# Performance work log

Measured on AMD Instinct MI355X. Metric: run time of the kernel, lower is better.

## Reference

```python
import jax, jax.numpy as jnp
import numpy as np

EPS = 0.5          # entropy_epsilon
TAU = 0.5          # tau = 1 * entropy_epsilon
MAXITER = 10

NABLA_W = np.array([[[[0., 0., 0.], [0., -1., 0.], [0., 1., 0.]]],
                    [[[0., 0., 0.], [0., -1., 1.], [0., 0., 0.]]]], dtype=np.float32)  # (2,1,3,3)
DIV_W = np.array([[[[0., -1., 0.], [0., 1., 0.], [0., 0., 0.]],
                   [[0., 0., 0.], [-1., 1., 0.], [0., 0., 0.]]]], dtype=np.float32)    # (1,2,3,3)


def _conv(x, w):
    # x: (B,C,H,W), w: (O,I,3,3), padding=1 -> SAME
    return jax.lax.conv_general_dilated(
        x, w, window_strides=(1, 1), padding='SAME',
        dimension_numbers=('NCHW', 'OIHW', 'NCHW'))


def setup_inputs() -> dict:
    key = jax.random.key(0)
    k1, k2 = jax.random.split(key)
    B, H, W = 8, 1024, 1024
    o = jax.random.normal(k1, (B, 1, H, W), dtype=jnp.float32)
    vector_field = jax.random.normal(k2, (H, W, 2), dtype=jnp.float32)
    nabla_w = jnp.asarray(NABLA_W)
    div_w = jnp.asarray(DIV_W)
    return {"o": o, "vector_field": vector_field, "nabla_w": nabla_w, "div_w": div_w}


def reference(o, vector_field, nabla_w, div_w):
    o = o[:, 0]                      # (B,H,W)
    vf1 = vector_field[:, :, 1]      # (H,W)
    vf0 = vector_field[:, :, 0]      # (H,W)
    u = jax.nn.sigmoid(o / EPS)
    q = jnp.zeros_like(o)
    Tq = jnp.zeros_like(o)
    for _ in range(MAXITER):
        u_nabla = _conv(u[:, None], nabla_w)          # (B,2,H,W)
        q = q - TAU * (u_nabla[:, 0] * vf1 + u_nabla[:, 1] * vf0)
        q = jnp.maximum(q, 0.0)
        Tq = _conv(jnp.stack([vf1 * q, vf0 * q], axis=1), div_w)[:, 0]  # (B,H,W)
        u = jax.nn.sigmoid((o - Tq) / EPS)
    u1 = (o - Tq) / EPS
    return u1
```

## Files before the change

### kernel.cpp

```cpp
#include <hip/hip_runtime.h>
#include <math.h>

#define IMG_H 1024
#define IMG_W 1024
#define IMG_B 8
#define TPB 512
#define PXT 2
#define RPB 16
#define BANDS (IMG_H / RPB)
#define NBLK (IMG_B * BANDS)

__device__ __forceinline__ float sig2(float x) {
    return 1.0f / (1.0f + __expf(-2.0f * x));
}
__device__ __forceinline__ int imax(int a, int b) { return a > b ? a : b; }
__device__ __forceinline__ int imin(int a, int b) { return a < b ? a : b; }

template<int D, bool READQ, bool FINAL>
__global__ __launch_bounds__(TPB, 4) void k_pipe(const float* __restrict__ qin,
                                                 const float* __restrict__ vf,
                                                 const float* __restrict__ o,
                                                 float* __restrict__ out) {
    __shared__ float sp[D + 1][TPB + 1];
    __shared__ float su[D][2][TPB + 1];

    const int img = blockIdx.x / BANDS;
    const int r0  = (blockIdx.x % BANDS) * RPB;
    const int tid = threadIdx.x;
    const int x0  = tid * PXT;
    const size_t ibase = (size_t)img * IMG_H * IMG_W;

    if (tid == 0) {
#pragma unroll
        for (int l = 0; l <= D; ++l) sp[l][0] = 0.0f;
#pragma unroll
        for (int l = 0; l < D; ++l) { su[l][0][TPB] = 0.0f; su[l][1][TPB] = 0.0f; }
    }

    constexpr int HALO = FINAL ? 1 : 0;
    constexpr int NOH  = FINAL ? D + 1 : D;

    const int u0lo = imax(r0 - (D - 1) - HALO, 0);
    const int ylo  = READQ ? imax(r0 - D - HALO, 0) : u0lo;
    const int yend = r0 + RPB - 1 + D;
    const int yhi  = imin(yend, IMG_H - 1);

    float qc[PXT], qn[PXT], qz[PXT];
    float oh[NOH][PXT], on[PXT];
    float v0h[D + 1][PXT], v1h[D + 1][PXT], v0n[PXT], v1n[PXT];
    float uY[D][PXT], uZ[D][PXT];
    float p1prev[D + 1][PXT];
    float qsave[D][PXT];
    float qvPrev[PXT];

#pragma unroll
    for (int j = 0; j < PXT; ++j) {
        qc[j]=qn[j]=qz[j]=on[j]=v0n[j]=v1n[j]=qvPrev[j]=0.0f;
#pragma unroll
        for (int l = 0; l < NOH; ++l) oh[l][j] = 0.0f;
#pragma unroll
        for (int l = 0; l <= D; ++l) { v0h[l][j]=0.0f; v1h[l][j]=0.0f; p1prev[l][j]=0.0f; }
#pragma unroll
        for (int l = 0; l < D; ++l) { uY[l][j]=0.0f; uZ[l][j]=0.0f; qsave[l][j]=0.0f; }
    }

    {
        const size_t rb = ibase + (size_t)ylo * IMG_W + x0;
        if constexpr (READQ) {
            float2 q2 = *(const float2*)(qin + rb);
            qc[0]=q2.x; qc[1]=q2.y;
        }
        float2 o2 = *(const float2*)(o + rb);
        oh[0][0]=o2.x; oh[0][1]=o2.y;
        const size_t vb = ((size_t)ylo * IMG_W + x0) * 2;
        float4 va = *(const float4*)(vf + vb);
        v0h[0][0]=va.x; v1h[0][0]=va.y; v0h[0][1]=va.z; v1h[0][1]=va.w;
    }

    for (int y = ylo; y <= yend; ++y) {
        if (y + 1 <= yhi) {
            const size_t rb = ibase + (size_t)(y + 1) * IMG_W + x0;
            if constexpr (READQ) {
                float2 q2 = *(const float2*)(qin + rb);
                qn[0]=q2.x; qn[1]=q2.y;
            }
            float2 o2 = *(const float2*)(o + rb);
            on[0]=o2.x; on[1]=o2.y;
            const size_t vb = ((size_t)(y + 1) * IMG_W + x0) * 2;
            float4 va = *(const float4*)(vf + vb);
            v0n[0]=va.x; v1n[0]=va.y; v0n[1]=va.z; v1n[1]=va.w;
        } else {
#pragma unroll
            for (int j = 0; j < PXT; ++j) { qn[j]=0.f; on[j]=0.f; v0n[j]=0.f; v1n[j]=0.f; }
        }

        if constexpr (READQ) {
            float p0c[PXT], p1c[PXT];
            const bool haveY = (y <= yhi);
            if (haveY) {
#pragma unroll
                for (int j = 0; j < PXT; ++j) { p0c[j]=v0h[0][j]*qc[j]; p1c[j]=v1h[0][j]*qc[j]; }
                sp[0][tid + 1] = p0c[PXT - 1];
            } else {
#pragma unroll
                for (int j = 0; j < PXT; ++j) { p0c[j]=0.f; p1c[j]=0.f; }
            }
            __syncthreads();
            if (y >= u0lo) {
                const float lft = sp[0][tid];
#pragma unroll
                for (int j = 0; j < PXT; ++j) {
                    float pm1 = (j == 0) ? lft : p0c[j - 1];
                    float nu = (y <= IMG_H - 1)
                        ? sig2(oh[0][j] - (p1c[j] - p1prev[0][j] + p0c[j] - pm1)) : 0.0f;
                    uZ[0][j] = uY[0][j]; uY[0][j] = nu;
                }
                su[0][y & 1][tid] = uY[0][0];
            }
#pragma unroll
            for (int j = 0; j < PXT; ++j) p1prev[0][j] = p1c[j];
        } else {
#pragma unroll
            for (int j = 0; j < PXT; ++j) {
                float nu = (y <= IMG_H - 1) ? sig2(oh[0][j]) : 0.0f;
                uZ[0][j] = uY[0][j]; uY[0][j] = nu;
            }
            su[0][y & 1][tid] = uY[0][0];
        }

#pragma unroll
        for (int l = 1; l <= D; ++l) {
            const int t = y - l;
            const int qlo = imax(r0 - (D - l) - HALO, 0);
            const bool qvalid = (t >= qlo) && (t <= IMG_H - 1);
            float qbase[PXT], qv[PXT];
#pragma unroll
            for (int j = 0; j < PXT; ++j)
                qbase[j] = (l == 1) ? (READQ ? qz[j] : 0.0f) : qsave[l - 1][j];
            if (l >= 2) {
#pragma unroll
                for (int j = 0; j < PXT; ++j) qsave[l - 1][j] = qvPrev[j];
            }
            if (qvalid) {
                const float uR = su[l - 1][t & 1][tid + 1];
#pragma unroll
                for (int j = 0; j < PXT; ++j) {
                    float gy = uY[l - 1][j] - uZ[l - 1][j];
                    float gx = ((j < PXT - 1) ? uZ[l - 1][j + 1] : uR) - uZ[l - 1][j];
                    qv[j] = fmaxf(qbase[j] - 0.5f * (gy * v1h[l][j] + gx * v0h[l][j]), 0.0f);
                }
            } else {
#pragma unroll
                for (int j = 0; j < PXT; ++j) qv[j] = 0.0f;
            }

            if (l < D) {
                float p0p[PXT], p1p[PXT];
                if (qvalid) {
#pragma unroll
                    for (int j = 0; j < PXT; ++j) { p0p[j]=v0h[l][j]*qv[j]; p1p[j]=v1h[l][j]*qv[j]; }
                    sp[l][tid + 1] = p0p[PXT - 1];
                } else {
#pragma unroll
                    for (int j = 0; j < PXT; ++j) { p0p[j]=0.f; p1p[j]=0.f; }
                }
                __syncthreads();
                const int ulo = imax(r0 - (D - 1 - l) - HALO, 0);
                if (t >= ulo) {
                    const float lft = sp[l][tid];
#pragma unroll
                    for (int j = 0; j < PXT; ++j) {
                        float pm1 = (j == 0) ? lft : p0p[j - 1];
                        float nu = (t <= IMG_H - 1)
                            ? sig2(oh[l][j] - (p1p[j] - p1prev[l][j] + p0p[j] - pm1)) : 0.0f;
                        uZ[l][j] = uY[l][j]; uY[l][j] = nu;
                    }
                    su[l][t & 1][tid] = uY[l][0];
                }
#pragma unroll
                for (int j = 0; j < PXT; ++j) p1prev[l][j] = p1p[j];
            } else {
                if constexpr (FINAL) {
                    float p0p[PXT], p1p[PXT];
                    if (qvalid) {
#pragma unroll
                        for (int j = 0; j < PXT; ++j) { p0p[j]=v0h[D][j]*qv[j]; p1p[j]=v1h[D][j]*qv[j]; }
                        sp[D][tid + 1] = p0p[PXT - 1];
                    } else {
#pragma unroll
                        for (int j = 0; j < PXT; ++j) { p0p[j]=0.f; p1p[j]=0.f; }
                    }
                    __syncthreads();
                    if (t >= r0 && t < r0 + RPB) {
                        const float lft = sp[D][tid];
                        float r[PXT];
#pragma unroll
                        for (int j = 0; j < PXT; ++j) {
                            float pm1 = (j == 0) ? lft : p0p[j - 1];
                            float Tq = p1p[j] - p1prev[D][j] + p0p[j] - pm1;
                            r[j] = 2.0f * (oh[D][j] - Tq);
                        }
                        *(float2*)(out + ibase + (size_t)t * IMG_W + x0) =
                            make_float2(r[0], r[1]);
                    }
#pragma unroll
                    for (int j = 0; j < PXT; ++j) p1prev[D][j] = p1p[j];
                } else {
                    if (t >= r0 && t < r0 + RPB) {
                        *(float2*)(out + ibase + (size_t)t * IMG_W + x0) =
                            make_float2(qv[0], qv[1]);
                    }
                }
            }
#pragma unroll
            for (int j = 0; j < PXT; ++j) qvPrev[j] = qv[j];
        }

#pragma unroll
        for (int k = D; k >= 1; --k)
#pragma unroll
            for (int j = 0; j < PXT; ++j) { v0h[k][j]=v0h[k-1][j]; v1h[k][j]=v1h[k-1][j]; }
#pragma unroll
        for (int j = 0; j < PXT; ++j) { v0h[0][j]=v0n[j]; v1h[0][j]=v1n[j]; }
#pragma unroll
        for (int k = NOH - 1; k >= 1; --k)
#pragma unroll
            for (int j = 0; j < PXT; ++j) oh[k][j] = oh[k-1][j];
#pragma unroll
        for (int j = 0; j < PXT; ++j) oh[0][j] = on[j];
        if constexpr (READQ) {
#pragma unroll
            for (int j = 0; j < PXT; ++j) { qz[j] = qc[j]; qc[j] = qn[j]; }
        }
    }
}

extern "C" void kernel_launch(void* const* d_in, const int* in_sizes, int n_in,
                              void* d_out, int out_size, void* d_ws, size_t ws_size,
                              hipStream_t stream) {
    const float* o  = (const float*)d_in[0];
    const float* vf = (const float*)d_in[1];
    float* qA = (float*)d_ws;

    k_pipe<5, false, false><<<NBLK, TPB, 0, stream>>>(o, vf, o, qA);
    k_pipe<5, true,  true ><<<NBLK, TPB, 0, stream>>>(qA, vf, o, (float*)d_out);
}
```

Baseline: 229.1 us.

## Use one pixel per thread with 1024-thread blocks and double-buffered shared rows

Each thread now handles one column pixel instead of two, so blocks grow to 1024 threads and the launch-bound occupancy hint doubles. The shared p buffer shrinks to two alternating rows, and the next-row register prefetch is dropped in favour of loading the current row directly through advancing pointers. The aim is more parallelism and fewer registers per thread. In exchange, loads become scalar rather than vector, more threads join each __syncthreads, and the load latency is no longer hidden by a one-row prefetch.

```diff
diff --git a/kernel.cpp b/kernel.cpp
--- a/kernel.cpp
+++ b/kernel.cpp
@@ -4,8 +4,7 @@
 #define IMG_H 1024
 #define IMG_W 1024
 #define IMG_B 8
-#define TPB 512
-#define PXT 2
+#define TPB 1024
 #define RPB 16
 #define BANDS (IMG_H / RPB)
 #define NBLK (IMG_B * BANDS)
@@ -17,22 +16,20 @@
 __device__ __forceinline__ int imin(int a, int b) { return a < b ? a : b; }
 
 template<int D, bool READQ, bool FINAL>
-__global__ __launch_bounds__(TPB, 4) void k_pipe(const float* __restrict__ qin,
+__global__ __launch_bounds__(TPB, 8) void k_pipe(const float* __restrict__ qin,
                                                  const float* __restrict__ vf,
                                                  const float* __restrict__ o,
                                                  float* __restrict__ out) {
-    __shared__ float sp[D + 1][TPB + 1];
+    __shared__ float sp[2][TPB + 1];
     __shared__ float su[D][2][TPB + 1];
 
     const int img = blockIdx.x / BANDS;
     const int r0  = (blockIdx.x % BANDS) * RPB;
     const int tid = threadIdx.x;
-    const int x0  = tid * PXT;
     const size_t ibase = (size_t)img * IMG_H * IMG_W;
 
     if (tid == 0) {
-#pragma unroll
-        for (int l = 0; l <= D; ++l) sp[l][0] = 0.0f;
+        sp[0][0] = 0.0f; sp[1][0] = 0.0f;
 #pragma unroll
         for (int l = 0; l < D; ++l) { su[l][0][TPB] = 0.0f; su[l][1][TPB] = 0.0f; }
     }
@@ -45,87 +42,58 @@
     const int yend = r0 + RPB - 1 + D;
     const int yhi  = imin(yend, IMG_H - 1);
 
-    float qc[PXT], qn[PXT], qz[PXT];
-    float oh[NOH][PXT], on[PXT];
-    float v0h[D + 1][PXT], v1h[D + 1][PXT], v0n[PXT], v1n[PXT];
-    float uY[D][PXT], uZ[D][PXT];
-    float p1prev[D + 1][PXT];
-    float qsave[D][PXT];
-    float qvPrev[PXT];
+    float qc = 0.0f, qz = 0.0f;
+    float oh[NOH];
+    float v0h[D + 1], v1h[D + 1];
+    float uY[D], uZ[D];
+    float p1prev[D + 1];
+    float qsave[D];
+    float qvPrev = 0.0f;
 
 #pragma unroll
-    for (int j = 0; j < PXT; ++j) {
-        qc[j]=qn[j]=qz[j]=on[j]=v0n[j]=v1n[j]=qvPrev[j]=0.0f;
+    for (int l = 0; l < NOH; ++l) oh[l] = 0.0f;
 #pragma unroll
-        for (int l = 0; l < NOH; ++l) oh[l][j] = 0.0f;
+    for (int l = 0; l <= D; ++l) { v0h[l] = 0.0f; v1h[l] = 0.0f; p1prev[l] = 0.0f; }
 #pragma unroll
-        for (int l = 0; l <= D; ++l) { v0h[l][j]=0.0f; v1h[l][j]=0.0f; p1prev[l][j]=0.0f; }
-#pragma unroll
-        for (int l = 0; l < D; ++l) { uY[l][j]=0.0f; uZ[l][j]=0.0f; qsave[l][j]=0.0f; }
-    }
+    for (int l = 0; l < D; ++l) { uY[l] = 0.0f; uZ[l] = 0.0f; qsave[l] = 0.0f; }
 
-    {
-        const size_t rb = ibase + (size_t)ylo * IMG_W + x0;
-        if constexpr (READQ) {
-            float2 q2 = *(const float2*)(qin + rb);
-            qc[0]=q2.x; qc[1]=q2.y;
-        }
-        float2 o2 = *(const float2*)(o + rb);
-        oh[0][0]=o2.x; oh[0][1]=o2.y;
-        const size_t vb = ((size_t)ylo * IMG_W + x0) * 2;
-        float4 va = *(const float4*)(vf + vb);
-        v0h[0][0]=va.x; v1h[0][0]=va.y; v0h[0][1]=va.z; v1h[0][1]=va.w;
-    }
+    const float* pQ = qin + ibase + (size_t)ylo * IMG_W + tid;
+    const float* pO = o   + ibase + (size_t)ylo * IMG_W + tid;
+    const float* pV = vf  + ((size_t)ylo * IMG_W + tid) * 2;
 
     for (int y = ylo; y <= yend; ++y) {
-        if (y + 1 <= yhi) {
-            const size_t rb = ibase + (size_t)(y + 1) * IMG_W + x0;
-            if constexpr (READQ) {
-                float2 q2 = *(const float2*)(qin + rb);
-                qn[0]=q2.x; qn[1]=q2.y;
-            }
-            float2 o2 = *(const float2*)(o + rb);
-            on[0]=o2.x; on[1]=o2.y;
-            const size_t vb = ((size_t)(y + 1) * IMG_W + x0) * 2;
-            float4 va = *(const float4*)(vf + vb);
-            v0n[0]=va.x; v1n[0]=va.y; v0n[1]=va.z; v1n[1]=va.w;
+#pragma unroll
+        for (int k = NOH - 1; k >= 1; --k) oh[k] = oh[k - 1];
+#pragma unroll
+        for (int k = D; k >= 1; --k) { v0h[k] = v0h[k - 1]; v1h[k] = v1h[k - 1]; }
+        if constexpr (READQ) qz = qc;
+
+        if (y <= yhi) {
+            if constexpr (READQ) { qc = *pQ; pQ += IMG_W; }
+            oh[0] = *pO; pO += IMG_W;
+            float2 v2 = *(const float2*)pV; pV += 2 * IMG_W;
+            v0h[0] = v2.x; v1h[0] = v2.y;
         } else {
-#pragma unroll
-            for (int j = 0; j < PXT; ++j) { qn[j]=0.f; on[j]=0.f; v0n[j]=0.f; v1n[j]=0.f; }
+            qc = 0.0f; oh[0] = 0.0f; v0h[0] = 0.0f; v1h[0] = 0.0f;
         }
 
         if constexpr (READQ) {
-            float p0c[PXT], p1c[PXT];
-            const bool haveY = (y <= yhi);
-            if (haveY) {
-#pragma unroll
-                for (int j = 0; j < PXT; ++j) { p0c[j]=v0h[0][j]*qc[j]; p1c[j]=v1h[0][j]*qc[j]; }
-                sp[0][tid + 1] = p0c[PXT - 1];
-            } else {
-#pragma unroll
-                for (int j = 0; j < PXT; ++j) { p0c[j]=0.f; p1c[j]=0.f; }
-            }
+            float p0c = v0h[0] * qc;
+            float p1c = v1h[0] * qc;
+            sp[0][tid + 1] = p0c;
             __syncthreads();
             if (y >= u0lo) {
-                const float lft = sp[0][tid];
-#pragma unroll
-                for (int j = 0; j < PXT; ++j) {
-                    float pm1 = (j == 0) ? lft : p0c[j - 1];
-                    float nu = (y <= IMG_H - 1)
-                        ? sig2(oh[0][j] - (p1c[j] - p1prev[0][j] + p0c[j] - pm1)) : 0.0f;
-                    uZ[0][j] = uY[0][j]; uY[0][j] = nu;
-                }
-                su[0][y & 1][tid] = uY[0][0];
+                float pm1 = sp[0][tid];
+                float nu = (y <= IMG_H - 1)
+                    ? sig2(oh[0] - (p1c - p1prev[0] + p0c - pm1)) : 0.0f;
+                uZ[0] = uY[0]; uY[0] = nu;
+                su[0][y & 1][tid] = nu;
             }
-#pragma unroll
-            for (int j = 0; j < PXT; ++j) p1prev[0][j] = p1c[j];
+            p1prev[0] = p1c;
         } else {
-#pragma unroll
-            for (int j = 0; j < PXT; ++j) {
-                float nu = (y <= IMG_H - 1) ? sig2(oh[0][j]) : 0.0f;
-                uZ[0][j] = uY[0][j]; uY[0][j] = nu;
-            }
-            su[0][y & 1][tid] = uY[0][0];
+            float nu = (y <= IMG_H - 1) ? sig2(oh[0]) : 0.0f;
+            uZ[0] = uY[0]; uY[0] = nu;
+            su[0][y & 1][tid] = nu;
         }
 
 #pragma unroll
@@ -133,104 +101,50 @@
             const int t = y - l;
             const int qlo = imax(r0 - (D - l) - HALO, 0);
             const bool qvalid = (t >= qlo) && (t <= IMG_H - 1);
-            float qbase[PXT], qv[PXT];
-#pragma unroll
-            for (int j = 0; j < PXT; ++j)
-                qbase[j] = (l == 1) ? (READQ ? qz[j] : 0.0f) : qsave[l - 1][j];
-            if (l >= 2) {
-#pragma unroll
-                for (int j = 0; j < PXT; ++j) qsave[l - 1][j] = qvPrev[j];
-            }
+            float qbase = (l == 1) ? (READQ ? qz : 0.0f) : qsave[l - 1];
+            if (l >= 2) qsave[l - 1] = qvPrev;
+            float qv;
             if (qvalid) {
                 const float uR = su[l - 1][t & 1][tid + 1];
-#pragma unroll
-                for (int j = 0; j < PXT; ++j) {
-                    float gy = uY[l - 1][j] - uZ[l - 1][j];
-                    float gx = ((j < PXT - 1) ? uZ[l - 1][j + 1] : uR) - uZ[l - 1][j];
-                    qv[j] = fmaxf(qbase[j] - 0.5f * (gy * v1h[l][j] + gx * v0h[l][j]), 0.0f);
-                }
+                float gy = uY[l - 1] - uZ[l - 1];
+                float gx = uR - uZ[l - 1];
+                qv = fmaxf(qbase - 0.5f * (gy * v1h[l] + gx * v0h[l]), 0.0f);
             } else {
-#pragma unroll
-                for (int j = 0; j < PXT; ++j) qv[j] = 0.0f;
+                qv = 0.0f;
             }
 
             if (l < D) {
-                float p0p[PXT], p1p[PXT];
-                if (qvalid) {
-#pragma unroll
-                    for (int j = 0; j < PXT; ++j) { p0p[j]=v0h[l][j]*qv[j]; p1p[j]=v1h[l][j]*qv[j]; }
-                    sp[l][tid + 1] = p0p[PXT - 1];
-                } else {
-#pragma unroll
-                    for (int j = 0; j < PXT; ++j) { p0p[j]=0.f; p1p[j]=0.f; }
-                }
+                float p0p = v0h[l] * qv;
+                float p1p = v1h[l] * qv;
+                sp[l & 1][tid + 1] = p0p;
                 __syncthreads();
                 const int ulo = imax(r0 - (D - 1 - l) - HALO, 0);
                 if (t >= ulo) {
-                    const float lft = sp[l][tid];
-#pragma unroll
-                    for (int j = 0; j < PXT; ++j) {
-                        float pm1 = (j == 0) ? lft : p0p[j - 1];
-                        float nu = (t <= IMG_H - 1)
-                            ? sig2(oh[l][j] - (p1p[j] - p1prev[l][j] + p0p[j] - pm1)) : 0.0f;
-                        uZ[l][j] = uY[l][j]; uY[l][j] = nu;
-                    }
-                    su[l][t & 1][tid] = uY[l][0];
+                    float pm1 = sp[l & 1][tid];
+                    float nu = (t <= IMG_H - 1)
+                        ? sig2(oh[l] - (p1p - p1prev[l] + p0p - pm1)) : 0.0f;
+                    uZ[l] = uY[l]; uY[l] = nu;
+                    su[l][t & 1][tid] = nu;
                 }
-#pragma unroll
-                for (int j = 0; j < PXT; ++j) p1prev[l][j] = p1p[j];
+                p1prev[l] = p1p;
             } else {
                 if constexpr (FINAL) {
-                    float p0p[PXT], p1p[PXT];
-                    if (qvalid) {
-#pragma unroll
-                        for (int j = 0; j < PXT; ++j) { p0p[j]=v0h[D][j]*qv[j]; p1p[j]=v1h[D][j]*qv[j]; }
-                        sp[D][tid + 1] = p0p[PXT - 1];
-                    } else {
-#pragma unroll
-                        for (int j = 0; j < PXT; ++j) { p0p[j]=0.f; p1p[j]=0.f; }
-                    }
+                    float p0p = v0h[D] * qv;
+                    float p1p = v1h[D] * qv;
+                    sp[D & 1][tid + 1] = p0p;
                     __syncthreads();
                     if (t >= r0 && t < r0 + RPB) {
-                        const float lft = sp[D][tid];
-                        float r[PXT];
-#pragma unroll
-                        for (int j = 0; j < PXT; ++j) {
-                            float pm1 = (j == 0) ? lft : p0p[j - 1];
-                            float Tq = p1p[j] - p1prev[D][j] + p0p[j] - pm1;
-                            r[j] = 2.0f * (oh[D][j] - Tq);
-                        }
-                        *(float2*)(out + ibase + (size_t)t * IMG_W + x0) =
-                            make_float2(r[0], r[1]);
+                        float pm1 = sp[D & 1][tid];
+                        float Tq = p1p - p1prev[D] + p0p - pm1;
+                        out[ibase + (size_t)t * IMG_W + tid] = 2.0f * (oh[D] - Tq);
                     }
-#pragma unroll
-                    for (int j = 0; j < PXT; ++j) p1prev[D][j] = p1p[j];
+                    p1prev[D] = p1p;
                 } else {
-                    if (t >= r0 && t < r0 + RPB) {
-                        *(float2*)(out + ibase + (size_t)t * IMG_W + x0) =
-                            make_float2(qv[0], qv[1]);
-                    }
+                    if (t >= r0 && t < r0 + RPB)
+                        out[ibase + (size_t)t * IMG_W + tid] = qv;
                 }
             }
-#pragma unroll
-            for (int j = 0; j < PXT; ++j) qvPrev[j] = qv[j];
-        }
-
-#pragma unroll
-        for (int k = D; k >= 1; --k)
-#pragma unroll
-            for (int j = 0; j < PXT; ++j) { v0h[k][j]=v0h[k-1][j]; v1h[k][j]=v1h[k-1][j]; }
-#pragma unroll
-        for (int j = 0; j < PXT; ++j) { v0h[0][j]=v0n[j]; v1h[0][j]=v1n[j]; }
-#pragma unroll
-        for (int k = NOH - 1; k >= 1; --k)
-#pragma unroll
-            for (int j = 0; j < PXT; ++j) oh[k][j] = oh[k-1][j];
-#pragma unroll
-        for (int j = 0; j < PXT; ++j) oh[0][j] = on[j];
-        if constexpr (READQ) {
-#pragma unroll
-            for (int j = 0; j < PXT; ++j) { qz[j] = qc[j]; qc[j] = qn[j]; }
+            qvPrev = qv;
         }
     }
 }
```

Result: faster. 218.0 us (-4.8%).
